# Optimization experiments

Hardware: AMD Instinct MI355X
Metric: run time of the kernel (lower is better)

Reference implementation:

```python
import jax, jax.numpy as jnp
import numpy as np

H = 4  # num_heads

def _ln(x, g, b):
    m = x.mean(-1, keepdims=True)
    v = ((x - m) ** 2).mean(-1, keepdims=True)
    return (x - m) * jax.lax.rsqrt(v + 1e-5) * g + b

def _mlp(x, w1, b1, w2, b2):
    return jax.nn.relu(x @ w1 + b1) @ w2 + b2

def _lin_att(q, k, v):
    # q,k,v: [BB, L, H, hd] ; linear (kernelized) attention, no softmax
    L = q.shape[1]
    qn = q / jnp.maximum(jnp.linalg.norm(q, axis=-1, keepdims=True), 1e-12)
    kn = k / jnp.maximum(jnp.linalg.norm(k, axis=-1, keepdims=True), 1e-12)
    kvs = jnp.einsum('blhm,blhd->bhmd', kn, v)
    num = jnp.einsum('bnhm,bhmd->bnhd', qn, kvs) + L * v
    den = jnp.einsum('bnhm,bhm->bnh', qn, kn.sum(axis=1))[..., None] + L
    return num / den

def _fast_attn(x4, w_qkv, w_op, b_op):
    # x4: [B,T,N,D]; spatial attention over N, temporal attention over T, concat, project
    B, T, N, D = x4.shape
    hd = D // H
    q, k, v = jnp.split(x4 @ w_qkv, 3, axis=-1)
    sh = lambda t: t.reshape(B * T, N, H, hd)
    out_s = _lin_att(sh(q), sh(k), sh(v)).reshape(B, T, N, D)
    th = lambda t: jnp.swapaxes(t, 1, 2).reshape(B * N, T, H, hd)
    out_t = jnp.swapaxes(_lin_att(th(q), th(k), th(v)).reshape(B, N, T, D), 1, 2)
    return jnp.concatenate([out_s, out_t], axis=-1) @ w_op + b_op

def _forward(x, W_in, b_in, adp, W_tp, b_tp, qkv_w, op_w, op_b, pw_w, pw_b,
             fc_w1, fc_b1, fc_w2, fc_b2, ln1_g, ln1_b, ln2_g, ln2_b,
             ep_w, ep_b, enc_w1, enc_b1, enc_w2, enc_b2, out_w, out_b):
    Nn, T, _ = x.shape
    xt = jnp.swapaxes(x, 0, 1)[None]                 # [1,T,N,in]
    h = xt @ W_in + b_in                             # input_proj -> [1,T,N,24]
    h = jnp.concatenate([h, adp[None]], axis=-1)     # + adaptive emb -> [1,T,N,104]
    h = h @ W_tp + b_tp                              # temporal_proj: 1x1 conv == pointwise linear
    graph = jnp.einsum('tnd,tmd->tnm', adp, adp)     # [T,N,N]
    graph = jax.nn.softmax(jax.nn.relu(graph), axis=-1)  # AvgPool(1,1) is identity
    # GraphPropagate (order=2, eval/no-dropout): [h, graph @ h]
    z1 = jnp.einsum('tni,btid->btnd', graph, h)
    att0 = _fast_attn(h, qkv_w[0], op_w[0], op_b[0])
    att1 = _fast_attn(z1, qkv_w[1], op_w[1], op_b[1])
    # scale = [1, 0.01]; note torch's in-place aliasing makes ln1 input = 2*x_glo
    g = h + att0 * (h @ pw_w[0] + pw_b[0]) + 0.01 * att1 * (att0 @ pw_w[1] + pw_b[1])
    h1 = _ln(2.0 * g, ln1_g, ln1_b)
    h2 = _ln(h1 + _mlp(h1, fc_w1, fc_b1, fc_w2, fc_b2), ln2_g, ln2_b)
    y = jnp.swapaxes(h2, 1, 2).reshape(1, Nn, T * h2.shape[-1]) @ ep_w + ep_b  # encoder_proj
    for i in range(enc_w1.shape[0]):                 # 3 residual MLP blocks
        y = y + _mlp(y, enc_w1[i], enc_b1[i], enc_w2[i], enc_b2[i])
    out = y @ out_w + out_b                          # [1,N,365]
    return out.reshape(Nn, T, 1)

def setup_inputs() -> dict:
    key = jax.random.key(0)
    ks = jax.random.split(key, 24)
    f = lambda i, shape, s=0.05: jax.random.normal(ks[i], shape, dtype=jnp.float32) * s
    D, T, N, IN = 104, 365, 400, 3
    return {
        'x': jax.random.normal(ks[0], (N, T, IN), dtype=jnp.float32),
        'W_in': f(1, (IN, 24)), 'b_in': f(2, (24,)),
        'adp': f(3, (T, N, 80)),
        'W_tp': f(4, (D, D)), 'b_tp': f(5, (D,)),
        'qkv_w': f(6, (2, D, 3 * D)),
        'op_w': f(7, (2, 2 * D, D)), 'op_b': f(8, (2, D)),
        'pw_w': f(9, (2, D, D)), 'pw_b': f(10, (2, D)),
        'fc_w1': f(11, (D, 2 * D)), 'fc_b1': f(12, (2 * D,)),
        'fc_w2': f(13, (2 * D, D)), 'fc_b2': f(14, (D,)),
        'ln1_g': jnp.ones((D,), jnp.float32), 'ln1_b': jnp.zeros((D,), jnp.float32),
        'ln2_g': jnp.ones((D,), jnp.float32), 'ln2_b': jnp.zeros((D,), jnp.float32),
        'ep_w': f(15, (T * D, D), 0.01), 'ep_b': f(16, (D,)),
        'enc_w1': f(17, (3, D, 2 * D)), 'enc_b1': f(18, (3, 2 * D)),
        'enc_w2': f(19, (3, 2 * D, D)), 'enc_b2': f(20, (3, D)),
        'out_w': f(21, (D, T)), 'out_b': f(22, (T,)),
    }

def reference(x, W_in, b_in, adp, W_tp, b_tp, qkv_w, op_w, op_b, pw_w, pw_b,
              fc_w1, fc_b1, fc_w2, fc_b2, ln1_g, ln1_b, ln2_g, ln2_b,
              ep_w, ep_b, enc_w1, enc_b1, enc_w2, enc_b2, out_w, out_b):
    return _forward(x, W_in, b_in, adp, W_tp, b_tp, qkv_w, op_w, op_b, pw_w, pw_b,
                    fc_w1, fc_b1, fc_w2, fc_b2, ln1_g, ln1_b, ln2_g, ln2_b,
                    ep_w, ep_b, enc_w1, enc_b1, enc_w2, enc_b2, out_w, out_b)
```

## Files before the change

kernel.cpp:

```cpp
#include <hip/hip_runtime.h>
#include <hip/hip_bf16.h>
#include <cstddef>

#define TT   365
#define NN   400
#define TN   (TT*NN)
#define HD   26
#define NH   4

#define CEILDIV(a,b) (((a)+(b)-1)/(b))

typedef __hip_bfloat16 bf16;
typedef short short8v __attribute__((ext_vector_type(8)));
typedef float float4v __attribute__((ext_vector_type(4)));
typedef float float16v __attribute__((ext_vector_type(16)));
__device__ __forceinline__ float b2f(bf16 v){ return __bfloat162float(v); }
__device__ __forceinline__ bf16  f2b(float v){ return __float2bfloat16(v); }

static constexpr size_t NB0 = (size_t)TN*104;
static constexpr size_t NB1 = (size_t)TN*104;
static constexpr size_t NB2 = (size_t)TN*312;
static constexpr size_t NB3 = (size_t)TN*104;
static constexpr size_t NBF = NB0+NB1+NB2+NB3;
static constexpr size_t NTILE   = (size_t)108*32;
static constexpr size_t NKVSB_S = (size_t)TT*NTILE;
static constexpr size_t NKVSB_T = (size_t)NN*NTILE;
static constexpr size_t NY      = (size_t)NN*104;
static constexpr size_t NW_TP   = 104*128;
static constexpr size_t NW_QKV  = 312*128;
static constexpr size_t NW_OP   = 104*224;
static constexpr size_t NW_PW   = 104*128;
static constexpr size_t NW_FC1  = 208*128;
static constexpr size_t NW_FC2  = 104*224;
static constexpr size_t NW_EPT  = (size_t)104*37960;
static constexpr size_t NWT     = NW_TP + 2*NW_QKV + 2*NW_OP + 2*NW_PW + NW_FC1 + NW_FC2 + NW_EPT;
static constexpr size_t WS_NEEDED = NBF*2 + (NKVSB_S+NKVSB_T)*2 + NY*4 + NWT*2;
static constexpr size_t NADP_ROWS = (size_t)TN + 64;
static constexpr size_t NADP = NADP_ROWS*96;
static constexpr size_t NHT  = ((size_t)TT*104 + 8)*448;
static_assert(NADP + NHT <= NB2, "z1 scratch must fit in B2");

__global__ void __launch_bounds__(256) prep_w(
    const float* __restrict__ W, bf16* __restrict__ Wt, int K, int Nc, int KP)
{
    int idx = blockIdx.x*256 + threadIdx.x;
    if (idx >= Nc*KP) return;
    int n = idx / KP, k = idx - n*KP;
    Wt[idx] = (k < K) ? f2b(W[(size_t)k*Nc + n]) : f2b(0.f);
}

__global__ void __launch_bounds__(256) prep_wT(
    const float* __restrict__ W, bf16* __restrict__ Wt)
{
    __shared__ float T[64][105];
    int k0 = blockIdx.x * 64;
    int tid = threadIdx.x;
    for (int idx = tid; idx < 64*104; idx += 256) {
        int r = idx / 104, c = idx - r*104;
        int k = k0 + r;
        T[r][c] = (k < 37960) ? W[(size_t)k*104 + c] : 0.f;
    }
    __syncthreads();
    for (int idx = tid; idx < 104*32; idx += 256) {
        int n = idx >> 5, kp = idx & 31;
        int k = kp*2;
        if (k0 + k + 1 < 37960 || k0 + k < 37960) {
            if (k0 + k < 37960) {
                bf16 lo = f2b(T[k][n]);
                bf16 hi = f2b(T[k+1][n]);
                uint v = ((uint)(*(ushort*)&hi) << 16) | (*(ushort*)&lo);
                if (k0 + k + 1 < 37960) *(uint*)(Wt + (size_t)n*37960 + k0 + k) = v;
                else Wt[(size_t)n*37960 + k0 + k] = lo;
            }
        }
    }
}

__global__ void __launch_bounds__(256) prep_adp(
    const float* __restrict__ adp, bf16* __restrict__ out)
{
    size_t i = (size_t)blockIdx.x*256 + threadIdx.x;
    if (i >= NADP) return;
    size_t row = i / 96; int e = (int)(i - row*96);
    float v = (row < TN && e < 80) ? adp[row*80 + e] : 0.f;
    out[i] = f2b(v);
}

__global__ void __launch_bounds__(256) ht_kernel(
    const bf16* __restrict__ h, bf16* __restrict__ hT)
{
    __shared__ bf16 As[64*106];
    int t = blockIdx.y, n0 = blockIdx.x*64;
    int tid = threadIdx.x;
    for (int idx = tid; idx < 64*52; idx += 256) {
        int r = idx / 52, k = idx - r*52;
        int n = n0 + r;
        uint v = 0;
        if (n < NN) v = *(const uint*)(h + ((size_t)t*NN + n)*104 + k*2);
        *(uint*)(&As[r*106 + k*2]) = v;
    }
    __syncthreads();
    for (int idx = tid; idx < 104*32; idx += 256) {
        int d = idx >> 5, np = idx & 31;
        int n = np*2;
        ushort lo = *(ushort*)&As[n*106 + d];
        ushort hi = *(ushort*)&As[(n+1)*106 + d];
        uint v = ((uint)hi << 16) | lo;
        *(uint*)(hT + ((size_t)t*104 + d)*448 + n0 + n) = v;
    }
}

__global__ void __launch_bounds__(256) hcat_kernel(
    const float* __restrict__ x, const float* __restrict__ W_in,
    const float* __restrict__ b_in, const float* __restrict__ adp,
    bf16* __restrict__ hcat)
{
    __shared__ bf16 T[16][112];
    int r0 = blockIdx.x * 16;
    int tid = threadIdx.x;
    for (int idx = tid; idx < 16*24; idx += 256) {
        int r = idx / 24, c = idx - r*24;
        int row = r0 + r;
        int t = row / NN, n = row - t*NN;
        size_t xb = ((size_t)n*TT + t)*3;
        float s = b_in[c] + x[xb]*W_in[c] + x[xb+1]*W_in[24+c] + x[xb+2]*W_in[48+c];
        T[r][c] = f2b(s);
    }
    for (int idx = tid; idx < 16*80; idx += 256) {
        int r = idx / 80, e = idx - r*80;
        T[r][24+e] = f2b(adp[(size_t)(r0+r)*80 + e]);
    }
    __syncthreads();
    for (int idx = tid; idx < 16*13; idx += 256) {
        int r = idx / 13, q = idx - r*13;
        *(uint4*)(hcat + ((size_t)(r0+r))*104 + q*8) = *(const uint4*)(&T[r][q*8]);
    }
}

template<int KP>
__global__ void __launch_bounds__(256) gemm_mf(
    const bf16* __restrict__ A, int lda, int K,
    const bf16* __restrict__ Wt, const float* __restrict__ bias,
    bf16* __restrict__ C, int M, int Nc, int relu)
{
    constexpr int STR = KP + 8;
    constexpr int KPQ = KP/8;
    __shared__ bf16 As[64*STR];
    __shared__ bf16 Ws[64*STR];
    int nCol = (Nc + 63) >> 6;
    int nwg = gridDim.x;
    int bid = blockIdx.x;
    int xcd = bid & 7, kk = bid >> 3;
    int q8 = nwg >> 3, r8 = nwg & 7;
    int widx = (xcd < r8 ? xcd*(q8+1) : r8*(q8+1) + (xcd - r8)*q8) + kk;
    int mblk = widx / nCol;
    int m0 = mblk * 64;
    int c0 = (widx - mblk*nCol) * 64;
    int tid = threadIdx.x;
    const int KQ = K/8;
    uint4 z4 = {0u,0u,0u,0u};
    for (int idx = tid; idx < 64*KPQ; idx += 256) {
        int r = idx / KPQ, q = idx - r*KPQ;
        int m = m0 + r;
        uint4 v = z4;
        if (m < M && q < KQ) v = *(const uint4*)(A + (size_t)m*lda + q*8);
        *(uint4*)(&As[r*STR + q*8]) = v;
    }
    for (int idx = tid; idx < 64*KPQ; idx += 256) {
        int r = idx / KPQ, q = idx - r*KPQ;
        int n = c0 + r;
        uint4 v = z4;
        if (n < Nc) v = *(const uint4*)(Wt + (size_t)n*KP + q*8);
        *(uint4*)(&Ws[r*STR + q*8]) = v;
    }
    __syncthreads();

    int lane = tid & 63, w = tid >> 6;
    int n16 = lane & 15, quad = lane >> 4;
    constexpr int KS = KP/32;
    short8v af[KS];
    #pragma unroll
    for (int s = 0; s < KS; ++s)
        af[s] = *(const short8v*)(&As[(16*w + n16)*STR + s*32 + quad*8]);
    float4v acc[4];
    #pragma unroll
    for (int ct = 0; ct < 4; ++ct) { float4v z = {0.f,0.f,0.f,0.f}; acc[ct] = z; }
    #pragma unroll
    for (int ct = 0; ct < 4; ++ct) {
        #pragma unroll
        for (int s = 0; s < KS; ++s) {
            short8v bfr = *(const short8v*)(&Ws[(ct*16 + n16)*STR + s*32 + quad*8]);
            acc[ct] = __builtin_amdgcn_mfma_f32_16x16x32_bf16(af[s], bfr, acc[ct], 0, 0, 0);
        }
    }
    #pragma unroll
    for (int ct = 0; ct < 4; ++ct) {
        int c = c0 + ct*16 + n16;
        if (c < Nc) {
            float b = bias ? bias[c] : 0.f;
            #pragma unroll
            for (int reg = 0; reg < 4; ++reg) {
                int m = m0 + 16*w + quad*4 + reg;
                if (m < M) {
                    float v = acc[ct][reg] + b;
                    if (relu) v = fmaxf(v, 0.f);
                    C[(size_t)m*Nc + c] = f2b(v);
                }
            }
        }
    }
}

__global__ void __launch_bounds__(256) gate_ln1(
    bf16* __restrict__ h, const bf16* __restrict__ att0, const bf16* __restrict__ att1,
    const bf16* __restrict__ w0t, const bf16* __restrict__ w1t, const float* __restrict__ pwb,
    const float* __restrict__ gamma, const float* __restrict__ beta)
{
    constexpr int STR = 136;
    __shared__ bf16 A0s[64*STR];
    __shared__ bf16 A1s[64*STR];
    __shared__ bf16 Ws[112*STR];
    __shared__ float prm[416];
    int m0 = blockIdx.x * 64;
    int tid = threadIdx.x;
    int lane = tid & 63, w = tid >> 6, n16 = lane & 15, quad = lane >> 4;
    uint4 z4 = {0u,0u,0u,0u};

    for (int idx = tid; idx < 64*16; idx += 256) {
        int r = idx >> 4, q = idx & 15;
        int m = m0 + r;
        uint4 v0 = z4, v1 = z4;
        if (m < TN && q < 13) {
            v0 = *(const uint4*)(h    + (size_t)m*104 + q*8);
            v1 = *(const uint4*)(att0 + (size_t)m*104 + q*8);
        }
        *(uint4*)(&A0s[r*STR + q*8]) = v0;
        *(uint4*)(&A1s[r*STR + q*8]) = v1;
    }
    for (int idx = tid; idx < 112*16; idx += 256) {
        int c = idx >> 4, q = idx & 15;
        uint4 v = z4;
        if (c < 104) v = *(const uint4*)(w0t + (size_t)c*128 + q*8);
        *(uint4*)(&Ws[c*STR + q*8]) = v;
    }
    for (int i = tid; i < 416; i += 256)
        prm[i] = (i < 208) ? pwb[i] : (i < 312 ? gamma[i-208] : beta[i-312]);
    __syncthreads();

    short8v a0f[4], a1f[4];
    #pragma unroll
    for (int s = 0; s < 4; ++s) {
        a0f[s] = *(const short8v*)(&A0s[(16*w + n16)*STR + s*32 + quad*8]);
        a1f[s] = *(const short8v*)(&A1s[(16*w + n16)*STR + s*32 + quad*8]);
    }
    float4v acc0[7], acc1[7];
    #pragma unroll
    for (int ct = 0; ct < 7; ++ct) { float4v z = {0.f,0.f,0.f,0.f}; acc0[ct] = z; acc1[ct] = z; }
    #pragma unroll
    for (int ct = 0; ct < 7; ++ct)
        #pragma unroll
        for (int s = 0; s < 4; ++s) {
            short8v bfr = *(const short8v*)(&Ws[(ct*16 + n16)*STR + s*32 + quad*8]);
            acc0[ct] = __builtin_amdgcn_mfma_f32_16x16x32_bf16(a0f[s], bfr, acc0[ct], 0, 0, 0);
        }
    __syncthreads();
    for (int idx = tid; idx < 112*16; idx += 256) {
        int c = idx >> 4, q = idx & 15;
        uint4 v = z4;
        if (c < 104) v = *(const uint4*)(w1t + (size_t)c*128 + q*8);
        *(uint4*)(&Ws[c*STR + q*8]) = v;
    }
    __syncthreads();
    #pragma unroll
    for (int ct = 0; ct < 7; ++ct)
        #pragma unroll
        for (int s = 0; s < 4; ++s) {
            short8v bfr = *(const short8v*)(&Ws[(ct*16 + n16)*STR + s*32 + quad*8]);
            acc1[ct] = __builtin_amdgcn_mfma_f32_16x16x32_bf16(a1f[s], bfr, acc1[ct], 0, 0, 0);
        }

    float sum[4] = {0.f,0.f,0.f,0.f};
    #pragma unroll
    for (int ct = 0; ct < 7; ++ct) {
        int c = ct*16 + n16;
        bool colok = c < 104;
        float b0 = colok ? prm[c] : 0.f;
        float b1 = colok ? prm[104 + c] : 0.f;
        #pragma unroll
        for (int reg = 0; reg < 4; ++reg) {
            int r = 16*w + quad*4 + reg;
            int m = m0 + r;
            float xv = 0.f;
            if (colok && m < TN) {
                float p0 = acc0[ct][reg] + b0;
                float p1 = acc1[ct][reg] + b1;
                float hv = b2f(A0s[r*STR + c]);
                float a0 = b2f(A1s[r*STR + c]);
                float a1 = b2f(att1[(size_t)m*104 + c]);
                xv = 2.f*(hv + a0*p0 + 0.01f*a1*p1);
            }
            acc0[ct][reg] = xv;
            sum[reg] += xv;
        }
    }
    #pragma unroll
    for (int reg = 0; reg < 4; ++reg) {
        float v = sum[reg];
        v += __shfl_xor(v,1,64); v += __shfl_xor(v,2,64);
        v += __shfl_xor(v,4,64); v += __shfl_xor(v,8,64);
        sum[reg] = v * (1.f/104.f);
    }
    float var[4] = {0.f,0.f,0.f,0.f};
    #pragma unroll
    for (int ct = 0; ct < 7; ++ct) {
        bool colok = (ct*16 + n16) < 104;
        #pragma unroll
        for (int reg = 0; reg < 4; ++reg) {
            if (colok) {
                float d = acc0[ct][reg] - sum[reg];
                acc0[ct][reg] = d;
                var[reg] += d*d;
            }
        }
    }
    #pragma unroll
    for (int reg = 0; reg < 4; ++reg) {
        float v = var[reg];
        v += __shfl_xor(v,1,64); v += __shfl_xor(v,2,64);
        v += __shfl_xor(v,4,64); v += __shfl_xor(v,8,64);
        var[reg] = rsqrtf(v * (1.f/104.f) + 1e-5f);
    }
    #pragma unroll
    for (int ct = 0; ct < 7; ++ct) {
        int c = ct*16 + n16;
        if (c < 104) {
            float g = prm[208 + c], be = prm[312 + c];
            #pragma unroll
            for (int reg = 0; reg < 4; ++reg) {
                int m = m0 + 16*w + quad*4 + reg;
                if (m < TN)
                    h[(size_t)m*104 + c] = f2b(acc0[ct][reg]*var[reg]*g + be);
            }
        }
    }
}

__global__ void __launch_bounds__(256) fc2_ln2(
    const bf16* __restrict__ hidden, const bf16* __restrict__ w2t, const float* __restrict__ b2,
    const bf16* __restrict__ h1, const float* __restrict__ gamma, const float* __restrict__ beta,
    bf16* __restrict__ h2)
{
    constexpr int STRA = 232;
    constexpr int STRW = 136;
    __shared__ bf16 As[64*STRA];
    __shared__ bf16 Ws[112*STRW];
    __shared__ float prm[312];
    int m0 = blockIdx.x * 64;
    int tid = threadIdx.x;
    int lane = tid & 63, w = tid >> 6, n16 = lane & 15, quad = lane >> 4;
    uint4 z4 = {0u,0u,0u,0u};

    for (int idx = tid; idx < 64*28; idx += 256) {
        int r = idx / 28, q = idx - r*28;
        int m = m0 + r;
        uint4 v = z4;
        if (m < TN && q < 26) v = *(const uint4*)(hidden + (size_t)m*208 + q*8);
        *(uint4*)(&As[r*STRA + q*8]) = v;
    }
    for (int idx = tid; idx < 112*16; idx += 256) {
        int c = idx >> 4, q = idx & 15;
        uint4 v = z4;
        if (c < 104) v = *(const uint4*)(w2t + (size_t)c*224 + q*8);
        *(uint4*)(&Ws[c*STRW + q*8]) = v;
    }
    for (int i = tid; i < 312; i += 256)
        prm[i] = (i < 104) ? b2[i] : (i < 208 ? gamma[i-104] : beta[i-208]);
    __syncthreads();

    short8v af[7];
    #pragma unroll
    for (int s = 0; s < 7; ++s)
        af[s] = *(const short8v*)(&As[(16*w + n16)*STRA + s*32 + quad*8]);
    float4v acc[7];
    #pragma unroll
    for (int ct = 0; ct < 7; ++ct) { float4v z = {0.f,0.f,0.f,0.f}; acc[ct] = z; }
    #pragma unroll
    for (int ct = 0; ct < 7; ++ct)
        #pragma unroll
        for (int s = 0; s < 4; ++s) {
            short8v bfr = *(const short8v*)(&Ws[(ct*16 + n16)*STRW + s*32 + quad*8]);
            acc[ct] = __builtin_amdgcn_mfma_f32_16x16x32_bf16(af[s], bfr, acc[ct], 0, 0, 0);
        }
    __syncthreads();
    for (int idx = tid; idx < 112*16; idx += 256) {
        int c = idx >> 4, q = idx & 15;
        uint4 v = z4;
        if (c < 104 && q < 12) v = *(const uint4*)(w2t + (size_t)c*224 + 128 + q*8);
        *(uint4*)(&Ws[c*STRW + q*8]) = v;
    }
    __syncthreads();
    #pragma unroll
    for (int ct = 0; ct < 7; ++ct)
        #pragma unroll
        for (int s = 4; s < 7; ++s) {
            short8v bfr = *(const short8v*)(&Ws[(ct*16 + n16)*STRW + (s-4)*32 + quad*8]);
            acc[ct] = __builtin_amdgcn_mfma_f32_16x16x32_bf16(af[s], bfr, acc[ct], 0, 0, 0);
        }

    float sum[4] = {0.f,0.f,0.f,0.f};
    #pragma unroll
    for (int ct = 0; ct < 7; ++ct) {
        int c = ct*16 + n16;
        bool colok = c < 104;
        float bb = colok ? prm[c] : 0.f;
        #pragma unroll
        for (int reg = 0; reg < 4; ++reg) {
            int m = m0 + 16*w + quad*4 + reg;
            float xv = 0.f;
            if (colok && m < TN)
                xv = b2f(h1[(size_t)m*104 + c]) + acc[ct][reg] + bb;
            acc[ct][reg] = xv;
            sum[reg] += xv;
        }
    }
    #pragma unroll
    for (int reg = 0; reg < 4; ++reg) {
        float v = sum[reg];
        v += __shfl_xor(v,1,64); v += __shfl_xor(v,2,64);
        v += __shfl_xor(v,4,64); v += __shfl_xor(v,8,64);
        sum[reg] = v * (1.f/104.f);
    }
    float var[4] = {0.f,0.f,0.f,0.f};
    #pragma unroll
    for (int ct = 0; ct < 7; ++ct) {
        bool colok = (ct*16 + n16) < 104;
        #pragma unroll
        for (int reg = 0; reg < 4; ++reg) {
            if (colok) {
                float d = acc[ct][reg] - sum[reg];
                acc[ct][reg] = d;
                var[reg] += d*d;
            }
        }
    }
    #pragma unroll
    for (int reg = 0; reg < 4; ++reg) {
        float v = var[reg];
        v += __shfl_xor(v,1,64); v += __shfl_xor(v,2,64);
        v += __shfl_xor(v,4,64); v += __shfl_xor(v,8,64);
        var[reg] = rsqrtf(v * (1.f/104.f) + 1e-5f);
    }
    #pragma unroll
    for (int ct = 0; ct < 7; ++ct) {
        int c = ct*16 + n16;
        if (c < 104) {
            float g = prm[104 + c], be = prm[208 + c];
            #pragma unroll
            for (int reg = 0; reg < 4; ++reg) {
                int m = m0 + 16*w + quad*4 + reg;
                if (m < TN)
                    h2[(size_t)m*104 + c] = f2b(acc[ct][reg]*var[reg]*g + be);
            }
        }
    }
}

__global__ void __launch_bounds__(256) ep_mf(
    const bf16* __restrict__ h2, const bf16* __restrict__ wt, float* __restrict__ y)
{
    constexpr int STR = 136;
    __shared__ bf16 As[64*STR];
    __shared__ bf16 Ws[64*STR];
    int m0 = blockIdx.x * 64;
    int c0 = blockIdx.y * 64;
    int t0 = blockIdx.z * 8;
    int t1 = min(TT, t0 + 8);
    int tid = threadIdx.x;
    int lane = tid & 63, w = tid >> 6, n16 = lane & 15, quad = lane >> 4;
    uint4 z4 = {0u,0u,0u,0u};

    float4v acc[4];
    #pragma unroll
    for (int ct = 0; ct < 4; ++ct) { float4v z = {0.f,0.f,0.f,0.f}; acc[ct] = z; }

    for (int t = t0; t < t1; ++t) {
        for (int idx = tid; idx < 64*16; idx += 256) {
            int r = idx >> 4, q = idx & 15;
            int m = m0 + r;
            uint4 va = z4;
            if (m < NN && q < 13) va = *(const uint4*)(h2 + ((size_t)t*NN + m)*104 + q*8);
            *(uint4*)(&As[r*STR + q*8]) = va;
            int c = c0 + r;
            uint4 vw = z4;
            if (c < 104 && q < 13) vw = *(const uint4*)(wt + (size_t)c*37960 + t*104 + q*8);
            *(uint4*)(&Ws[r*STR + q*8]) = vw;
        }
        __syncthreads();
        short8v af[4];
        #pragma unroll
        for (int s = 0; s < 4; ++s)
            af[s] = *(const short8v*)(&As[(16*w + n16)*STR + s*32 + quad*8]);
        #pragma unroll
        for (int ct = 0; ct < 4; ++ct) {
            #pragma unroll
            for (int s = 0; s < 4; ++s) {
                short8v bfr = *(const short8v*)(&Ws[(ct*16 + n16)*STR + s*32 + quad*8]);
                acc[ct] = __builtin_amdgcn_mfma_f32_16x16x32_bf16(af[s], bfr, acc[ct], 0, 0, 0);
            }
        }
        __syncthreads();
    }
    #pragma unroll
    for (int ct = 0; ct < 4; ++ct) {
        int c = c0 + ct*16 + n16;
        if (c < 104) {
            #pragma unroll
            for (int reg = 0; reg < 4; ++reg) {
                int m = m0 + 16*w + quad*4 + reg;
                if (m < NN) atomicAdd(&y[(size_t)m*104 + c], acc[ct][reg]);
            }
        }
    }
}

static constexpr int Z1_TQ = CEILDIV(TT, 8);
static constexpr int Z1_BLOCKS = 8 * Z1_TQ * 4;
__global__ void __launch_bounds__(512, 4) z1_mf(
    const bf16* __restrict__ adp_bf, const bf16* __restrict__ hT, bf16* __restrict__ z1)
{
    constexpr int SA  = 104;
    constexpr int SH  = 72;
    constexpr int SPP = 72;
    __shared__ bf16 Asq[2][64*SA];
    __shared__ bf16 Bt[64*SA];
    __shared__ bf16 Hs[128*SH];
    __shared__ bf16 P[2][64*SPP];
    __shared__ float rsb[2][2][64];

    int bid = blockIdx.x;
    int xcd = bid & 7;
    int j = bid >> 3;
    int tq = j >> 2, pair = j & 3;
    int t = tq*8 + xcd;
    if (t >= TT) return;

    int tid = threadIdx.x;
    int lane = tid & 63, w = tid >> 6;
    int slab = w >> 2, wsl = w & 3;
    int qi = wsl >> 1, ci = wsl & 1;
    int n32 = lane & 31, koct = lane >> 5;
    int r0 = (pair*2 + slab)*64;

    {
        const uint4* src = (const uint4*)(adp_bf + ((size_t)t*NN + pair*128)*96);
        #pragma unroll
        for (int i = 0; i < 3; ++i) {
            int idx = tid + i*512;
            int s2 = idx / 768, rem = idx - s2*768;
            int r = rem / 12, q = rem - r*12;
            *(uint4*)(&Asq[s2][r*SA + q*8]) = src[idx];
        }
    }
    {
        uint4 z4v = {0u,0u,0u,0u};
        for (int idx = tid; idx < 216; idx += 512) {
            int rr = idx / 9;
            int r = 104 + rr, q = idx - rr*9;
            *(uint4*)(&Hs[r*SH + q*8]) = z4v;
        }
    }

    float16v on0, on1;
    #pragma unroll
    for (int i = 0; i < 16; ++i) { on0[i] = 0.f; on1[i] = 0.f; }
    float rs2[16];
    #pragma unroll
    for (int i = 0; i < 16; ++i) rs2[i] = 0.f;

    const bf16* hbase = hT + (size_t)t*104*448;

    uint4 preB0, preB1, preH0, preH1;
    {
        const uint4* srcB = (const uint4*)(adp_bf + (size_t)t*NN*96);
        preB0 = srcB[tid];
        if (tid < 256) preB1 = srcB[tid + 512];
        { int r = tid >> 3, q = tid & 7;
          preH0 = *(const uint4*)(hbase + (size_t)r*448 + q*8); }
        if (tid < 320) { int idx = tid + 512; int r = idx >> 3, q = idx & 7;
          preH1 = *(const uint4*)(hbase + (size_t)r*448 + q*8); }
    }

    for (int c0 = 0; c0 < NN; c0 += 64) {
        { int r = tid / 12, q = tid - (tid/12)*12;
          *(uint4*)(&Bt[r*SA + q*8]) = preB0; }
        if (tid < 256) { int idx = tid + 512; int r = idx / 12, q = idx - r*12;
          *(uint4*)(&Bt[r*SA + q*8]) = preB1; }
        { int r = tid >> 3, q = tid & 7;
          *(uint4*)(&Hs[r*SH + q*8]) = preH0; }
        if (tid < 320) { int idx = tid + 512; int r = idx >> 3, q = idx & 7;
          *(uint4*)(&Hs[r*SH + q*8]) = preH1; }
        __syncthreads();
        int cn = c0 + 64;
        if (cn < NN) {
            const uint4* srcB = (const uint4*)(adp_bf + ((size_t)t*NN + cn)*96);
            preB0 = srcB[tid];
            if (tid < 256) preB1 = srcB[tid + 512];
            { int r = tid >> 3, q = tid & 7;
              preH0 = *(const uint4*)(hbase + (size_t)r*448 + cn + q*8); }
            if (tid < 320) { int idx = tid + 512; int r = idx >> 3, q = idx & 7;
              preH1 = *(const uint4*)(hbase + (size_t)r*448 + cn + q*8); }
        }
        float16v sc;
        #pragma unroll
        for (int i = 0; i < 16; ++i) sc[i] = 0.f;
        #pragma unroll
        for (int s = 0; s < 6; ++s) {
            short8v afq = *(const short8v*)(&Asq[slab][(qi*32 + n32)*SA + s*16 + koct*8]);
            short8v bfr = *(const short8v*)(&Bt[(ci*32 + n32)*SA + s*16 + koct*8]);
            sc = __builtin_amdgcn_mfma_f32_32x32x16_bf16(afq, bfr, sc, 0, 0, 0);
        }
        bool colok = (c0 + ci*32 + n32) < NN;
        #pragma unroll
        for (int reg = 0; reg < 16; ++reg) {
            int crow = (reg & 3) + 8*(reg >> 2) + 4*koct;
            float e = colok ? __expf(fmaxf(sc[reg], 0.f)) : 0.f;
            rs2[reg] += e;
            P[slab][(qi*32 + crow)*SPP + ci*32 + n32] = f2b(e);
        }
        __syncthreads();
        short8v pA[4];
        #pragma unroll
        for (int s = 0; s < 4; ++s)
            pA[s] = *(const short8v*)(&P[slab][(qi*32 + n32)*SPP + s*16 + koct*8]);
        #pragma unroll
        for (int s = 0; s < 4; ++s) {
            short8v hb0 = *(const short8v*)(&Hs[(ci*32 + n32)*SH + s*16 + koct*8]);
            on0 = __builtin_amdgcn_mfma_f32_32x32x16_bf16(pA[s], hb0, on0, 0, 0, 0);
        }
        #pragma unroll
        for (int s = 0; s < 4; ++s) {
            short8v hb1 = *(const short8v*)(&Hs[((ci+2)*32 + n32)*SH + s*16 + koct*8]);
            on1 = __builtin_amdgcn_mfma_f32_32x32x16_bf16(pA[s], hb1, on1, 0, 0, 0);
        }
        __syncthreads();
    }

    #pragma unroll
    for (int reg = 0; reg < 16; ++reg) {
        float v = rs2[reg];
        v += __shfl_xor(v, 1, 64);
        v += __shfl_xor(v, 2, 64);
        v += __shfl_xor(v, 4, 64);
        v += __shfl_xor(v, 8, 64);
        v += __shfl_xor(v, 16, 64);
        if (n32 == 0) {
            int crow = (reg & 3) + 8*(reg >> 2) + 4*koct;
            rsb[slab][ci][qi*32 + crow] = v;
        }
    }
    __syncthreads();

    #pragma unroll
    for (int reg = 0; reg < 16; ++reg) {
        int crow = (reg & 3) + 8*(reg >> 2) + 4*koct;
        int qrow = qi*32 + crow;
        int gq = r0 + qrow;
        if (gq < NN) {
            float inv = 1.f / (rsb[slab][0][qrow] + rsb[slab][1][qrow]);
            int d0 = ci*32 + n32;
            z1[((size_t)t*NN + gq)*104 + d0] = f2b(on0[reg] * inv);
            int d1 = (ci + 2)*32 + n32;
            if (d1 < 104)
                z1[((size_t)t*NN + gq)*104 + d1] = f2b(on1[reg] * inv);
        }
    }
}

__global__ void __launch_bounds__(256) kvs_mf(
    const bf16* __restrict__ qkv, bf16* __restrict__ kvsb_s, bf16* __restrict__ kvsb_t)
{
    constexpr int CK = 32;
    constexpr int TS = 40;
    __shared__ bf16 raw[CK][216];
    __shared__ bf16 kTn[4][32][TS];
    __shared__ bf16 vT [4][32][TS];
    __shared__ float invs[CK][4];

    int bb = blockIdx.x;
    bf16* out; int L; long long strideL, base;
    if (bb < TT) { out = kvsb_s + (size_t)bb*NTILE; L = NN; base = (long long)bb*NN*312 + 104; strideL = 312; }
    else { int n = bb - TT; out = kvsb_t + (size_t)n*NTILE; L = TT; base = (long long)n*312 + 104; strideL = (long long)NN*312; }

    int tid = threadIdx.x;
    int lane = tid & 63, w = tid >> 6;
    int n32 = lane & 31, koct = lane >> 5;
    uint4 z4 = {0u,0u,0u,0u};

    float16v acc;
    #pragma unroll
    for (int i = 0; i < 16; ++i) acc[i] = 0.f;

    uint4 pre[4];
    #pragma unroll
    for (int j = 0; j < 4; ++j) {
        int idx = tid + j*256;
        uint4 v = z4;
        if (idx < CK*26) {
            int r = idx / 26, q = idx - r*26;
            if (r < L) v = *(const uint4*)(qkv + base + (long long)r*strideL + q*8);
        }
        pre[j] = v;
    }

    for (int l0 = 0; l0 < L; l0 += CK) {
        int lw = min(CK, L - l0);
        __syncthreads();
        #pragma unroll
        for (int j = 0; j < 4; ++j) {
            int idx = tid + j*256;
            if (idx < CK*26) {
                int r = idx / 26, q = idx - r*26;
                *(uint4*)(&raw[r][q*8]) = pre[j];
            }
        }
        __syncthreads();
        {
            int ln0 = l0 + CK;
            #pragma unroll
            for (int j = 0; j < 4; ++j) {
                int idx = tid + j*256;
                uint4 v = z4;
                if (idx < CK*26 && ln0 < L) {
                    int r = idx / 26, q = idx - r*26;
                    if (r < L - ln0) v = *(const uint4*)(qkv + base + (long long)(ln0 + r)*strideL + q*8);
                }
                pre[j] = v;
            }
        }
        if (tid < CK*4) {
            int l = tid >> 2, h = tid & 3;
            float ss = 0.f;
            #pragma unroll
            for (int m = 0; m < HD; ++m) { float v = b2f(raw[l][h*HD + m]); ss += v*v; }
            invs[l][h] = (l < lw) ? 1.f/fmaxf(sqrtf(ss), 1e-12f) : 0.f;
        }
        __syncthreads();
        for (int idx = tid; idx < 4*CK*HD; idx += 256) {
            int h = idx / (CK*HD); int rem = idx - h*CK*HD;
            int l = rem / HD; int m = rem - l*HD;
            float iv = invs[l][h];
            kTn[h][m][l] = f2b(b2f(raw[l][h*HD + m]) * iv);
            vT[h][m][l]  = raw[l][104 + h*HD + m];
        }
        if (tid < 4*CK) {
            int h = tid >> 5, l = tid & 31;
            vT[h][26][l] = f2b((l < lw) ? 1.f : 0.f);
        }
        __syncthreads();
        #pragma unroll
        for (int s = 0; s < 2; ++s) {
            short8v a = *(const short8v*)(&kTn[w][n32][s*16 + koct*8]);
            short8v b = *(const short8v*)(&vT [w][n32][s*16 + koct*8]);
            acc = __builtin_amdgcn_mfma_f32_32x32x16_bf16(a, b, acc, 0, 0, 0);
        }
    }

    int lo = w*HD;
    #pragma unroll
    for (int reg = 0; reg < 16; ++reg) {
        int m = (reg & 3) + 8*(reg >> 2) + 4*koct;
        if (m < HD) {
            if (n32 < HD)       out[(size_t)(lo + n32)*32 + m] = f2b(acc[reg]);
            else if (n32 == HD) out[(size_t)(104 + w)*32 + m] = f2b(acc[reg]);
        }
    }
}

__global__ void __launch_bounds__(256) attn_mm(
    bf16* __restrict__ qkv, const bf16* __restrict__ kvsb,
    int M, long long bStride, long long rowStride, float Lf, int outOff)
{
    constexpr int STR = 136;
    __shared__ bf16 As[64*STR];
    __shared__ bf16 Ws[112*STR];
    __shared__ float nsqL[64*4];
    __shared__ float denL[64*4];
    int mt = blockIdx.x, bb = blockIdx.y;
    int tid = threadIdx.x;
    int lane = tid & 63, w = tid >> 6, n16 = lane & 15, quad = lane >> 4;
    bf16* base = qkv + (size_t)bb * bStride;
    int r0 = mt*64;
    uint4 z4 = {0u,0u,0u,0u};

    for (int idx = tid; idx < 64*16; idx += 256) {
        int r = idx >> 4, q = idx & 15;
        int m = r0 + r;
        uint4 v = z4;
        if (m < M && q < 13) v = *(const uint4*)(base + (size_t)m*rowStride + q*8);
        *(uint4*)(&As[r*STR + q*8]) = v;
    }
    for (int idx = tid; idx < 112*16; idx += 256) {
        int c = idx >> 4, q = idx & 15;
        *(uint4*)(&Ws[c*STR + q*8]) = z4;
    }
    __syncthreads();
    {
        const bf16* kb = kvsb + (size_t)bb * NTILE;
        for (int idx = tid; idx < 108*13; idx += 256) {
            int c = idx / 13, qu = idx - c*13;
            int lo = (c < 104) ? (c/26)*26 : (c-104)*26;
            *(uint*)(&Ws[c*STR + lo + qu*2]) = *(const uint*)(kb + (size_t)c*32 + qu*2);
        }
    }
    __syncthreads();

    short8v af[4];
    #pragma unroll
    for (int s = 0; s < 4; ++s)
        af[s] = *(const short8v*)(&As[(16*w + n16)*STR + s*32 + quad*8]);
    float4v acc[7];
    #pragma unroll
    for (int ct = 0; ct < 7; ++ct) { float4v z = {0.f,0.f,0.f,0.f}; acc[ct] = z; }
    #pragma unroll
    for (int ct = 0; ct < 7; ++ct) {
        #pragma unroll
        for (int s = 0; s < 4; ++s) {
            short8v bfr = *(const short8v*)(&Ws[(ct*16 + n16)*STR + s*32 + quad*8]);
            acc[ct] = __builtin_amdgcn_mfma_f32_16x16x32_bf16(af[s], bfr, acc[ct], 0, 0, 0);
        }
    }
    {
        int row = tid >> 2, hh = tid & 3;
        const bf16* qr = &As[row*STR + hh*26];
        float ss = 0.f;
        #pragma unroll
        for (int m = 0; m < HD; ++m) { float v = b2f(qr[m]); ss += v*v; }
        nsqL[row*4 + hh] = ss;
    }
    if (n16 >= 8 && n16 < 12) {
        #pragma unroll
        for (int reg = 0; reg < 4; ++reg)
            denL[(16*w + quad*4 + reg)*4 + (n16 - 8)] = acc[6][reg];
    }
    __syncthreads();
    #pragma unroll
    for (int ct = 0; ct < 7; ++ct) {
        int c = ct*16 + n16;
        if (c < 104) {
            int hh = c / 26;
            #pragma unroll
            for (int reg = 0; reg < 4; ++reg) {
                int lr = 16*w + quad*4 + reg;
                int m = r0 + lr;
                if (m < M) {
                    float iq = 1.f / fmaxf(sqrtf(nsqL[lr*4 + hh]), 1e-12f);
                    float den = iq * denL[lr*4 + hh] + Lf;
                    bf16* rp = base + (size_t)m*rowStride;
                    float num = iq * acc[ct][reg] + Lf * b2f(rp[208 + c]);
                    rp[outOff + c] = f2b(num / den);
                }
            }
        }
    }
}

__global__ void __launch_bounds__(256) y_init_kernel(float* __restrict__ y, const float* __restrict__ ep_b) {
    int i = blockIdx.x*256 + threadIdx.x;
    if (i < NN*104) y[i] = ep_b[i % 104];
}

__global__ void __launch_bounds__(256) tail_kernel(
    const float* __restrict__ y,
    const float* __restrict__ ew1, const float* __restrict__ eb1,
    const float* __restrict__ ew2, const float* __restrict__ eb2,
    const float* __restrict__ out_w, const float* __restrict__ out_b,
    float* __restrict__ out)
{
    int n0 = blockIdx.x * 2;
    int tid = threadIdx.x;
    __shared__ float yr[2][104], hid[2][208];
    if (tid < 104) {
        yr[0][tid] = y[(size_t)n0*104 + tid];
        yr[1][tid] = y[(size_t)(n0+1)*104 + tid];
    }
    __syncthreads();
    for (int i = 0; i < 3; ++i) {
        const float* w1 = ew1 + (size_t)i*104*208;
        const float* b1 = eb1 + (size_t)i*208;
        const float* w2 = ew2 + (size_t)i*208*104;
        const float* b2 = eb2 + (size_t)i*104;
        if (tid < 208) {
            float a0 = b1[tid], a1 = a0;
            #pragma unroll 8
            for (int k = 0; k < 104; ++k) {
                float w = w1[(size_t)k*208 + tid];
                a0 += yr[0][k]*w; a1 += yr[1][k]*w;
            }
            hid[0][tid] = fmaxf(a0, 0.f);
            hid[1][tid] = fmaxf(a1, 0.f);
        }
        __syncthreads();
        float y0 = 0.f, y1 = 0.f;
        if (tid < 104) {
            float a0 = b2[tid], a1 = a0;
            #pragma unroll 8
            for (int k = 0; k < 208; ++k) {
                float w = w2[(size_t)k*104 + tid];
                a0 += hid[0][k]*w; a1 += hid[1][k]*w;
            }
            y0 = yr[0][tid] + a0; y1 = yr[1][tid] + a1;
        }
        __syncthreads();
        if (tid < 104) { yr[0][tid] = y0; yr[1][tid] = y1; }
        __syncthreads();
    }
    for (int t = tid; t < TT; t += 256) {
        float a0 = out_b[t], a1 = a0;
        #pragma unroll 8
        for (int d = 0; d < 104; ++d) {
            float w = out_w[(size_t)d*TT + t];
            a0 += yr[0][d]*w; a1 += yr[1][d]*w;
        }
        out[(size_t)n0*TT + t] = a0;
        out[(size_t)(n0+1)*TT + t] = a1;
    }
}

extern "C" void kernel_launch(void* const* d_in, const int* in_sizes, int n_in,
                              void* d_out, int out_size, void* d_ws, size_t ws_size,
                              hipStream_t stream) {
    if (ws_size < WS_NEEDED) return;

    const float* x      = (const float*)d_in[0];
    const float* W_in   = (const float*)d_in[1];
    const float* b_in   = (const float*)d_in[2];
    const float* adp    = (const float*)d_in[3];
    const float* W_tp   = (const float*)d_in[4];
    const float* b_tp   = (const float*)d_in[5];
    const float* qkv_w  = (const float*)d_in[6];
    const float* op_w   = (const float*)d_in[7];
    const float* op_b   = (const float*)d_in[8];
    const float* pw_w   = (const float*)d_in[9];
    const float* pw_b   = (const float*)d_in[10];
    const float* fc_w1  = (const float*)d_in[11];
    const float* fc_b1  = (const float*)d_in[12];
    const float* fc_w2  = (const float*)d_in[13];
    const float* fc_b2  = (const float*)d_in[14];
    const float* ln1_g  = (const float*)d_in[15];
    const float* ln1_b  = (const float*)d_in[16];
    const float* ln2_g  = (const float*)d_in[17];
    const float* ln2_b  = (const float*)d_in[18];
    const float* ep_w   = (const float*)d_in[19];
    const float* ep_b   = (const float*)d_in[20];
    const float* enc_w1 = (const float*)d_in[21];
    const float* enc_b1 = (const float*)d_in[22];
    const float* enc_w2 = (const float*)d_in[23];
    const float* enc_b2 = (const float*)d_in[24];
    const float* out_w  = (const float*)d_in[25];
    const float* out_b  = (const float*)d_in[26];

    bf16* B0 = (bf16*)d_ws;
    bf16* B1 = B0 + NB0;
    bf16* B2 = B1 + NB1;
    bf16* B3 = B2 + NB2;
    bf16* kvsb_s = B3 + NB3;
    bf16* kvsb_t = kvsb_s + NKVSB_S;
    float* ybuf  = (float*)(kvsb_t + NKVSB_T);
    bf16* wtp   = (bf16*)(ybuf + NY);
    bf16* wqkv0 = wtp + NW_TP;
    bf16* wqkv1 = wqkv0 + NW_QKV;
    bf16* wop0  = wqkv1 + NW_QKV;
    bf16* wop1  = wop0 + NW_OP;
    bf16* wpw0  = wop1 + NW_OP;
    bf16* wpw1  = wpw0 + NW_PW;
    bf16* wfc1  = wpw1 + NW_PW;
    bf16* wfc2  = wfc1 + NW_FC1;
    bf16* wept  = wfc2 + NW_FC2;
    bf16* adp_bf = B2;
    bf16* hTbuf  = B2 + NADP;

    prep_w<<<CEILDIV(104*128,256), 256, 0, stream>>>(W_tp, wtp, 104, 104, 128);
    prep_w<<<CEILDIV(312*128,256), 256, 0, stream>>>(qkv_w, wqkv0, 104, 312, 128);
    prep_w<<<CEILDIV(312*128,256), 256, 0, stream>>>(qkv_w + 104*312, wqkv1, 104, 312, 128);
    prep_w<<<CEILDIV(104*224,256), 256, 0, stream>>>(op_w, wop0, 208, 104, 224);
    prep_w<<<CEILDIV(104*224,256), 256, 0, stream>>>(op_w + 208*104, wop1, 208, 104, 224);
    prep_w<<<CEILDIV(104*128,256), 256, 0, stream>>>(pw_w, wpw0, 104, 104, 128);
    prep_w<<<CEILDIV(104*128,256), 256, 0, stream>>>(pw_w + 104*104, wpw1, 104, 104, 128);
    prep_w<<<CEILDIV(208*128,256), 256, 0, stream>>>(fc_w1, wfc1, 104, 208, 128);
    prep_w<<<CEILDIV(104*224,256), 256, 0, stream>>>(fc_w2, wfc2, 208, 104, 224);
    prep_wT<<<CEILDIV(37960,64), 256, 0, stream>>>(ep_w, wept);

    const int GX = CEILDIV(TN, 64);

    hcat_kernel<<<CEILDIV(TN,16), 256, 0, stream>>>(x, W_in, b_in, adp, B2);
    gemm_mf<128><<<GX*2, 256, 0, stream>>>(B2, 104, 104, wtp, b_tp, B0, TN, 104, 0);
    prep_adp<<<CEILDIV((int)NADP,256), 256, 0, stream>>>(adp, adp_bf);
    ht_kernel<<<dim3(7, TT), 256, 0, stream>>>(B0, hTbuf);
    z1_mf<<<Z1_BLOCKS, 512, 0, stream>>>(adp_bf, hTbuf, B1);
    gemm_mf<128><<<GX*5, 256, 0, stream>>>(B0, 104, 104, wqkv0, nullptr, B2, TN, 312, 0);
    kvs_mf<<<TT+NN, 256, 0, stream>>>(B2, kvsb_s, kvsb_t);
    attn_mm<<<dim3(6, NN), 256, 0, stream>>>(B2, kvsb_t, TT, 312, (long long)NN*312, (float)TT, 104);
    attn_mm<<<dim3(7, TT), 256, 0, stream>>>(B2, kvsb_s, NN, (long long)NN*312, 312, (float)NN, 0);
    gemm_mf<224><<<GX*2, 256, 0, stream>>>(B2, 312, 208, wop0, op_b, B3, TN, 104, 0);
    gemm_mf<128><<<GX*5, 256, 0, stream>>>(B1, 104, 104, wqkv1, nullptr, B2, TN, 312, 0);
    kvs_mf<<<TT+NN, 256, 0, stream>>>(B2, kvsb_s, kvsb_t);
    attn_mm<<<dim3(6, NN), 256, 0, stream>>>(B2, kvsb_t, TT, 312, (long long)NN*312, (float)TT, 104);
    attn_mm<<<dim3(7, TT), 256, 0, stream>>>(B2, kvsb_s, NN, (long long)NN*312, 312, (float)NN, 0);
    gemm_mf<224><<<GX*2, 256, 0, stream>>>(B2, 312, 208, wop1, op_b + 104, B1, TN, 104, 0);
    gate_ln1<<<GX, 256, 0, stream>>>(B0, B3, B1, wpw0, wpw1, pw_b, ln1_g, ln1_b);
    gemm_mf<128><<<GX*4, 256, 0, stream>>>(B0, 104, 104, wfc1, fc_b1, B2, TN, 208, 1);
    fc2_ln2<<<GX, 256, 0, stream>>>(B2, wfc2, fc_b2, B0, ln2_g, ln2_b, B3);
    y_init_kernel<<<CEILDIV(NN*104,256), 256, 0, stream>>>(ybuf, ep_b);
    ep_mf<<<dim3(CEILDIV(NN,64), 2, CEILDIV(TT,8)), 256, 0, stream>>>(B3, wept, ybuf);
    tail_kernel<<<NN/2, 256, 0, stream>>>(ybuf, enc_w1, enc_b1, enc_w2, enc_b2,
                                          out_w, out_b, (float*)d_out);
}
```

Measured before the change: 1.254 ms.

## Fuse spatial linear attention with output projection GEMM

Adds an attn_op kernel that computes the spatial linear-attention output for a 64-row tile into shared memory. It then immediately multiplies the concatenated spatial and temporal attention rows by the output projection weights, adding bias. This replaces the separate spatial attn_mm launch and the gemm_mf<224> output projection for both branches. It avoids writing the spatial attention result to global memory and reading the 208-wide concat back, at the cost of larger shared-memory use per block and serialized weight staging within the kernel.

Result: faster. 1.215 ms (-3.1%).

```diff
diff --git a/kernel.cpp b/kernel.cpp
--- a/kernel.cpp
+++ b/kernel.cpp
@@ -859,6 +859,148 @@
                     float num = iq * acc[ct][reg] + Lf * b2f(rp[208 + c]);
                     rp[outOff + c] = f2b(num / den);
                 }
+            }
+        }
+    }
+}
+
+__global__ void __launch_bounds__(256) attn_op(
+    const bf16* __restrict__ qkv, const bf16* __restrict__ kvsb,
+    const bf16* __restrict__ wt, const float* __restrict__ bias,
+    bf16* __restrict__ Cout, float Lf)
+{
+    constexpr int SA = 232;
+    constexpr int SW = 136;
+    __shared__ bf16 Acat[64*SA];
+    __shared__ bf16 Ws[112*SW];
+    __shared__ float nsqL[64*4];
+    __shared__ float denL[64*4];
+    int mt = blockIdx.x, t = blockIdx.y;
+    int tid = threadIdx.x;
+    int lane = tid & 63, w = tid >> 6, n16 = lane & 15, quad = lane >> 4;
+    const bf16* base = qkv + (size_t)t * ((size_t)NN*312);
+    int r0 = mt*64;
+    uint4 z4 = {0u,0u,0u,0u};
+
+    for (int idx = tid; idx < 64*29; idx += 256) {
+        int r = idx / 29, q = idx - r*29;
+        int m = r0 + r;
+        uint4 v = z4;
+        if (m < NN && q < 26) v = *(const uint4*)(base + (size_t)m*312 + q*8);
+        *(uint4*)(&Acat[r*SA + q*8]) = v;
+    }
+    for (int idx = tid; idx < 112*16; idx += 256) {
+        int c = idx >> 4, q = idx & 15;
+        *(uint4*)(&Ws[c*SW + q*8]) = z4;
+    }
+    __syncthreads();
+    {
+        const bf16* kb = kvsb + (size_t)t * NTILE;
+        for (int idx = tid; idx < 108*13; idx += 256) {
+            int c = idx / 13, qu = idx - c*13;
+            int lo = (c < 104) ? (c/26)*26 : (c-104)*26;
+            *(uint*)(&Ws[c*SW + lo + qu*2]) = *(const uint*)(kb + (size_t)c*32 + qu*2);
+        }
+    }
+    __syncthreads();
+
+    short8v af[4];
+    #pragma unroll
+    for (int s = 0; s < 4; ++s)
+        af[s] = *(const short8v*)(&Acat[(16*w + n16)*SA + s*32 + quad*8]);
+    float4v acc[7];
+    #pragma unroll
+    for (int ct = 0; ct < 7; ++ct) { float4v z = {0.f,0.f,0.f,0.f}; acc[ct] = z; }
+    #pragma unroll
+    for (int ct = 0; ct < 7; ++ct) {
+        #pragma unroll
+        for (int s = 0; s < 4; ++s) {
+            short8v bfr = *(const short8v*)(&Ws[(ct*16 + n16)*SW + s*32 + quad*8]);
+            acc[ct] = __builtin_amdgcn_mfma_f32_16x16x32_bf16(af[s], bfr, acc[ct], 0, 0, 0);
+        }
+    }
+    {
+        int row = tid >> 2, hh = tid & 3;
+        const bf16* qr = &Acat[row*SA + hh*26];
+        float ss = 0.f;
+        #pragma unroll
+        for (int m = 0; m < HD; ++m) { float v = b2f(qr[m]); ss += v*v; }
+        nsqL[row*4 + hh] = ss;
+    }
+    if (n16 >= 8 && n16 < 12) {
+        #pragma unroll
+        for (int reg = 0; reg < 4; ++reg)
+            denL[(16*w + quad*4 + reg)*4 + (n16 - 8)] = acc[6][reg];
+    }
+    __syncthreads();
+
+    #pragma unroll
+    for (int ct = 0; ct < 7; ++ct) {
+        int c = ct*16 + n16;
+        if (c < 104) {
+            int hh = c / 26;
+            #pragma unroll
+            for (int reg = 0; reg < 4; ++reg) {
+                int lr = 16*w + quad*4 + reg;
+                int m = r0 + lr;
+                if (m < NN) {
+                    float iq = 1.f / fmaxf(sqrtf(nsqL[lr*4 + hh]), 1e-12f);
+                    float den = iq * denL[lr*4 + hh] + Lf;
+                    const bf16* rp = base + (size_t)m*312;
+                    float num = iq * acc[ct][reg] + Lf * b2f(rp[208 + c]);
+                    Acat[lr*SA + c] = f2b(num / den);
+                }
+            }
+        }
+    }
+    for (int idx = tid; idx < 112*16; idx += 256) {
+        int c = idx >> 4, q = idx & 15;
+        uint4 v = z4;
+        if (c < 104) v = *(const uint4*)(wt + (size_t)c*224 + q*8);
+        *(uint4*)(&Ws[c*SW + q*8]) = v;
+    }
+    __syncthreads();
+
+    short8v af2[7];
+    #pragma unroll
+    for (int s = 0; s < 7; ++s)
+        af2[s] = *(const short8v*)(&Acat[(16*w + n16)*SA + s*32 + quad*8]);
+    float4v acc2[7];
+    #pragma unroll
+    for (int ct = 0; ct < 7; ++ct) { float4v z = {0.f,0.f,0.f,0.f}; acc2[ct] = z; }
+    #pragma unroll
+    for (int ct = 0; ct < 7; ++ct)
+        #pragma unroll
+        for (int s = 0; s < 4; ++s) {
+            short8v bfr = *(const short8v*)(&Ws[(ct*16 + n16)*SW + s*32 + quad*8]);
+            acc2[ct] = __builtin_amdgcn_mfma_f32_16x16x32_bf16(af2[s], bfr, acc2[ct], 0, 0, 0);
+        }
+    __syncthreads();
+    for (int idx = tid; idx < 112*16; idx += 256) {
+        int c = idx >> 4, q = idx & 15;
+        uint4 v = z4;
+        if (c < 104 && q < 12) v = *(const uint4*)(wt + (size_t)c*224 + 128 + q*8);
+        *(uint4*)(&Ws[c*SW + q*8]) = v;
+    }
+    __syncthreads();
+    #pragma unroll
+    for (int ct = 0; ct < 7; ++ct)
+        #pragma unroll
+        for (int s = 4; s < 7; ++s) {
+            short8v bfr = *(const short8v*)(&Ws[(ct*16 + n16)*SW + (s-4)*32 + quad*8]);
+            acc2[ct] = __builtin_amdgcn_mfma_f32_16x16x32_bf16(af2[s], bfr, acc2[ct], 0, 0, 0);
+        }
+
+    #pragma unroll
+    for (int ct = 0; ct < 7; ++ct) {
+        int c = ct*16 + n16;
+        if (c < 104) {
+            float b = bias[c];
+            #pragma unroll
+            for (int reg = 0; reg < 4; ++reg) {
+                int m = r0 + 16*w + quad*4 + reg;
+                if (m < NN)
+                    Cout[((size_t)t*NN + m)*104 + c] = f2b(acc2[ct][reg] + b);
             }
         }
     }
@@ -1000,13 +1142,11 @@
     gemm_mf<128><<<GX*5, 256, 0, stream>>>(B0, 104, 104, wqkv0, nullptr, B2, TN, 312, 0);
     kvs_mf<<<TT+NN, 256, 0, stream>>>(B2, kvsb_s, kvsb_t);
     attn_mm<<<dim3(6, NN), 256, 0, stream>>>(B2, kvsb_t, TT, 312, (long long)NN*312, (float)TT, 104);
-    attn_mm<<<dim3(7, TT), 256, 0, stream>>>(B2, kvsb_s, NN, (long long)NN*312, 312, (float)NN, 0);
-    gemm_mf<224><<<GX*2, 256, 0, stream>>>(B2, 312, 208, wop0, op_b, B3, TN, 104, 0);
+    attn_op<<<dim3(7, TT), 256, 0, stream>>>(B2, kvsb_s, wop0, op_b, B3, (float)NN);
     gemm_mf<128><<<GX*5, 256, 0, stream>>>(B1, 104, 104, wqkv1, nullptr, B2, TN, 312, 0);
     kvs_mf<<<TT+NN, 256, 0, stream>>>(B2, kvsb_s, kvsb_t);
     attn_mm<<<dim3(6, NN), 256, 0, stream>>>(B2, kvsb_t, TT, 312, (long long)NN*312, (float)TT, 104);
-    attn_mm<<<dim3(7, TT), 256, 0, stream>>>(B2, kvsb_s, NN, (long long)NN*312, 312, (float)NN, 0);
-    gemm_mf<224><<<GX*2, 256, 0, stream>>>(B2, 312, 208, wop1, op_b + 104, B1, TN, 104, 0);
+    attn_op<<<dim3(7, TT), 256, 0, stream>>>(B2, kvsb_s, wop1, op_b + 104, B1, (float)NN);
     gate_ln1<<<GX, 256, 0, stream>>>(B0, B3, B1, wpw0, wpw1, pw_b, ln1_g, ln1_b);
     gemm_mf<128><<<GX*4, 256, 0, stream>>>(B0, 104, 104, wfc1, fc_b1, B2, TN, 208, 1);
     fc2_ln2<<<GX, 256, 0, stream>>>(B2, wfc2, fc_b2, B0, ln2_g, ln2_b, B3);
```
